# Optimization experiments

Hardware: AMD Instinct MI355X
Metric: run time of the kernel (lower is better)

The kernel has to match this reference:

```python
import jax, jax.numpy as jnp
import numpy as np

EPS = 1e-5

def mean_variance_norm(x):
    # x: [b, c, h, w]; per-(b,c) instance norm over spatial, unbiased var (torch default)
    b, c, h, w = x.shape
    xf = x.reshape(b, c, h * w)
    mean = xf.mean(axis=2)
    var = xf.var(axis=2, ddof=1) + EPS
    std = jnp.sqrt(var)
    return (x - mean[:, :, None, None]) / std[:, :, None, None]

def conv1x1(x, w, b):
    # w: [out_c, in_c], b: [out_c]
    return jnp.einsum('oc,bchw->bohw', w, x) + b[None, :, None, None]

def setup_inputs() -> dict:
    key = jax.random.key(0)
    ks = jax.random.split(key, 10)
    b, C, H, W = 4, 512, 64, 64
    content = jax.random.normal(ks[0], (b, C, H, W), dtype=jnp.float32)
    style = jax.random.normal(ks[1], (b, C, H, W), dtype=jnp.float32)
    def w_(k, o, i):
        return jax.random.normal(k, (o, i), dtype=jnp.float32) * 0.02
    def b_(k, o):
        return jax.random.normal(k, (o,), dtype=jnp.float32) * 0.02
    return {
        'content': content, 'style': style,
        'f_w': w_(ks[2], C, C), 'f_b': b_(ks[3], C),
        'g_w': w_(ks[4], C, C), 'g_b': b_(ks[5], C),
        'h_w': w_(ks[6], C, C), 'h_b': b_(ks[7], C),
        'out_w': w_(ks[8], C, C), 'out_b': b_(ks[9], C),
    }

def reference(content, style, f_w, f_b, g_w, g_b, h_w, h_b, out_w, out_b):
    b, C, h, w = content.shape
    F = conv1x1(mean_variance_norm(content), f_w, f_b)   # [b,C,h,w]
    G = conv1x1(mean_variance_norm(style), g_w, g_b)     # [b,C,hg,wg]
    H = conv1x1(style, h_w, h_b)                          # [b,C,hg,wg]
    # spatial <= max_sample, so no subsampling branch
    Gf = G.reshape(b, C, -1)                              # [b,C,M]
    Hf = H.reshape(b, C, -1)                              # [b,C,M]
    Ff = F.reshape(b, C, -1)                              # [b,C,N]
    S = jnp.einsum('bcn,bcm->bnm', Ff, Gf)                # [b,N,M]
    S = jax.nn.softmax(S, axis=-1)
    styled = jnp.einsum('bcm,bnm->bcn', Hf, S)            # [b,C,N]
    styled = styled.reshape(b, C, h, w)
    return conv1x1(styled, out_w, out_b)
```

## Files before the change

kernel.cpp:

```cpp
#include <hip/hip_runtime.h>
#include <hip/hip_bf16.h>

typedef _Float16 f16;
typedef __attribute__((ext_vector_type(8))) _Float16 half8;
typedef __attribute__((ext_vector_type(4))) _Float16 half4;
typedef __attribute__((ext_vector_type(4))) float f32x4;

#define AS1 __attribute__((address_space(1)))
#define AS3 __attribute__((address_space(3)))

constexpr int CH  = 512;
constexpr int NSP = 4096;
constexpr int NB  = 4;

#define VM8  asm volatile("s_waitcnt vmcnt(8)"  ::: "memory")
#define VM6  asm volatile("s_waitcnt vmcnt(6)"  ::: "memory")
#define VM4  asm volatile("s_waitcnt vmcnt(4)"  ::: "memory")
#define VM2  asm volatile("s_waitcnt vmcnt(2)"  ::: "memory")
#define VM0  asm volatile("s_waitcnt vmcnt(0)"  ::: "memory")
#define BARS do { __builtin_amdgcn_s_barrier(); asm volatile("" ::: "memory"); } while (0)
#define SP1  __builtin_amdgcn_s_setprio(1)
#define SP0  __builtin_amdgcn_s_setprio(0)

__device__ __forceinline__ void gload_lds16(const void* g, void* l) {
    __builtin_amdgcn_global_load_lds((const AS1 void*)g, (AS3 void*)l, 16, 0, 0);
}

__global__ void transpose_f16_kernel(const float* __restrict__ content, const float* __restrict__ style,
                                     f16* __restrict__ content_t, f16* __restrict__ style_t,
                                     float* __restrict__ raw)
{
    int b = blockIdx.z & 3, is_style = blockIdx.z >> 2;
    const float* src = (is_style ? style : content) + (size_t)b * CH * NSP;
    f16* dst = (is_style ? style_t : content_t) + (size_t)b * NSP * CH;
    int c0 = blockIdx.y * 64, n0 = blockIdx.x * 64;
    __shared__ f16 tile[64][72];
    int t = threadIdx.x;
    #pragma unroll
    for (int i = 0; i < 4; i++) {
        int idx = t + i*256;
        int cr = idx >> 4, n4 = (idx & 15) * 4;
        float4 v = *(const float4*)(src + (size_t)(c0+cr)*NSP + n0 + n4);
        tile[cr][n4+0] = (f16)v.x; tile[cr][n4+1] = (f16)v.y;
        tile[cr][n4+2] = (f16)v.z; tile[cr][n4+3] = (f16)v.w;
    }
    __syncthreads();
    {
        int row = t >> 2, seg = (t & 3) * 16;
        float s1 = 0.f, s2 = 0.f;
        #pragma unroll
        for (int j = 0; j < 16; j++) {
            float x = (float)tile[row][seg + j];
            s1 += x; s2 += x * x;
        }
        s1 += __shfl_down(s1, 2, 4); s1 += __shfl_down(s1, 1, 4);
        s2 += __shfl_down(s2, 2, 4); s2 += __shfl_down(s2, 1, 4);
        if ((t & 3) == 0) {
            int si = is_style * 2 * NB * CH + b * CH + c0 + row;
            atomicAdd(&raw[si], s1);
            atomicAdd(&raw[si + NB * CH], s2);
        }
    }
    int nr = t >> 2, seg = (t & 3) * 16;
    __align__(16) f16 out_v[16];
    #pragma unroll
    for (int j = 0; j < 16; j++) out_v[j] = tile[seg + j][nr];
    f16* dp = dst + (size_t)(n0+nr)*CH + c0 + seg;
    *(int4*)dp = ((int4*)out_v)[0];
    *(int4*)(dp + 8) = ((int4*)out_v)[1];
}

__global__ void effw_kernel(const float* __restrict__ fw, const float* __restrict__ fb,
                            const float* __restrict__ gw, const float* __restrict__ gb,
                            const float* __restrict__ hw, const float* __restrict__ ow,
                            const float* __restrict__ raw,
                            f16* __restrict__ fw_e, float* __restrict__ fb_e,
                            f16* __restrict__ gw_e, float* __restrict__ gb_e,
                            f16* __restrict__ hw_h, f16* __restrict__ ow_h)
{
    int o = blockIdx.x, b = blockIdx.y, mode = blockIdx.z, t = threadIdx.x;
    if (mode >= 2) {
        if (b != 0) return;
        const float* srcw = (mode == 2) ? hw : ow;
        f16* dstw = (mode == 2) ? hw_h : ow_h;
        for (int c = t; c < CH; c += 128) dstw[o*CH + c] = (f16)srcw[o*CH + c];
        return;
    }
    const float* w  = mode ? gw : fw;
    const float* rw = raw + (mode ? 2*NB*CH : 0);
    f16* we = mode ? gw_e : fw_e;
    float part = 0.f;
    for (int c = t; c < CH; c += 128) {
        float s1 = rw[b*CH + c], s2 = rw[NB*CH + b*CH + c];
        float mn = s1 * (1.f/NSP);
        float var = (s2 - (float)NSP*mn*mn) * (1.f/(NSP-1));
        float is = rsqrtf(var + 1e-5f);
        float wv = w[o*CH + c];
        we[((size_t)b*CH + o)*CH + c] = (f16)(wv * is);
        part += wv * mn * is;
    }
    #pragma unroll
    for (int off = 32; off; off >>= 1) part += __shfl_down(part, off);
    __shared__ float rr[2];
    if ((t & 63) == 0) rr[t >> 6] = part;
    __syncthreads();
    if (t == 0) (mode ? gb_e : fb_e)[b*CH + o] = (mode ? gb : fb)[o] - (rr[0] + rr[1]);
}

__global__ __launch_bounds__(256)
void conv3_kernel(const f16* __restrict__ fw_e, const float* __restrict__ fb_e,
                  const f16* __restrict__ gw_e, const float* __restrict__ gb_e,
                  const f16* __restrict__ hw_h, const float* __restrict__ h_b,
                  const f16* __restrict__ content_t, const f16* __restrict__ style_t,
                  f16* __restrict__ F_t, f16* __restrict__ G_t, f16* __restrict__ H_)
{
    const int T = gridDim.x;
    const int bid = blockIdx.x;
    const int tile = (bid & 7) * (T >> 3) + (bid >> 3);
    const int zz = tile >> 7, rem = tile & 127;
    const int mt = rem >> 5, nt = rem & 31;
    const int kind = zz >> 2, b = zz & 3;

    const f16* W; const float* bias; const f16* Xt; f16* Y;
    if (kind == 0)      { W = fw_e + (size_t)b*CH*CH; bias = fb_e + b*CH; Xt = content_t + (size_t)b*NSP*CH; Y = F_t + (size_t)b*NSP*CH; }
    else if (kind == 1) { W = gw_e + (size_t)b*CH*CH; bias = gb_e + b*CH; Xt = style_t + (size_t)b*NSP*CH; Y = G_t + (size_t)b*NSP*CH; }
    else                { W = hw_h;                    bias = h_b;         Xt = style_t + (size_t)b*NSP*CH; Y = H_ + (size_t)b*CH*NSP; }

    const int m0 = mt * 128, n0 = nt * 128;
    const int t = threadIdx.x, wave = t >> 6, lane = t & 63;
    const int l15 = lane & 15, l4 = lane >> 4;
    const int wm = (wave >> 1) * 64, wn = (wave & 1) * 64;

    __shared__ __align__(16) f16 Al[8192];
    __shared__ __align__(16) f16 Bl[8192];

    f32x4 acc[4][4] = {};

    for (int ks = 0; ks < CH/64; ks++) {
        const int kk = ks * 64;
        #pragma unroll
        for (int j = 0; j < 4; j++) {
            int L  = ((wave*4 + j)*64 + lane) * 16;
            int SL = L ^ (((L >> 7) & 7) << 4);
            int row = SL >> 7, seg = (SL & 127) >> 1;
            gload_lds16(W  + (size_t)(m0 + row)*CH + kk + seg, &Al[L >> 1]);
            gload_lds16(Xt + (size_t)(n0 + row)*CH + kk + seg, &Bl[L >> 1]);
        }
        VM0; BARS;
        #pragma unroll
        for (int kb = 0; kb < 2; kb++) {
            half8 a[4], bb[4];
            #pragma unroll
            for (int i = 0; i < 4; i++) {
                int ab = (wm + i*16 + l15)*128 + kb*64 + l4*16;
                ab ^= ((ab >> 7) & 7) << 4;
                a[i] = *(const half8*)&Al[ab >> 1];
                int bby = (wn + i*16 + l15)*128 + kb*64 + l4*16;
                bby ^= ((bby >> 7) & 7) << 4;
                bb[i] = *(const half8*)&Bl[bby >> 1];
            }
            #pragma unroll
            for (int i = 0; i < 4; i++)
                #pragma unroll
                for (int jj = 0; jj < 4; jj++)
                    acc[i][jj] = __builtin_amdgcn_mfma_f32_16x16x32_f16(a[i], bb[jj], acc[i][jj], 0, 0, 0);
        }
        BARS;
    }

    #pragma unroll
    for (int i = 0; i < 4; i++) {
        const int ob = m0 + wm + i*16 + l4*4;
        f32x4 bv = *(const f32x4*)(bias + ob);
        #pragma unroll
        for (int jj = 0; jj < 4; jj++) {
            const int n = n0 + wn + jj*16 + l15;
            f32x4 v = acc[i][jj];
            v[0] += bv[0]; v[1] += bv[1]; v[2] += bv[2]; v[3] += bv[3];
            if (kind < 2) {
                half4 pk; pk[0]=(f16)v[0]; pk[1]=(f16)v[1]; pk[2]=(f16)v[2]; pk[3]=(f16)v[3];
                *(half4*)(Y + (size_t)n * CH + ob) = pk;
            } else {
                #pragma unroll
                for (int r = 0; r < 4; r++) Y[(size_t)(ob + r) * NSP + n] = (f16)v[r];
            }
        }
    }
}

template<int MODE>
__global__ __launch_bounds__(256)
void gemm_kernel(const f16* __restrict__ W, long wstrideb,
                 const f16* __restrict__ Xt, long xstrideb,
                 const float* __restrict__ bias, long bstrideb,
                 void* __restrict__ Y, long ystrideb,
                 int K, long ostride)
{
    const int z = blockIdx.z;
    W    += (size_t)z * wstrideb;
    Xt   += (size_t)z * xstrideb;
    bias += (size_t)z * bstrideb;
    const int m0 = blockIdx.y * 128, n0 = blockIdx.x * 128;
    const int t = threadIdx.x, wave = t >> 6, lane = t & 63;
    const int l15 = lane & 15, l4 = lane >> 4;
    const int wm = (wave >> 1) * 64, wn = (wave & 1) * 64;

    __shared__ __align__(16) f16 Al[2][8192];
    __shared__ __align__(16) f16 Bl[2][8192];

    f32x4 acc[4][4] = {};

    auto stage = [&](int bufi, int kk) {
        #pragma unroll
        for (int j = 0; j < 4; j++) {
            int L  = ((wave*4 + j)*64 + lane) * 16;
            int SL = L ^ (((L >> 7) & 7) << 4);
            int row = SL >> 7, seg = (SL & 127) >> 1;
            gload_lds16(W  + (size_t)(m0 + row)*K + kk + seg, &Al[bufi][L >> 1]);
            gload_lds16(Xt + (size_t)(n0 + row)*K + kk + seg, &Bl[bufi][L >> 1]);
        }
    };

    const int nks = K >> 6;
    stage(0, 0);
    for (int ks = 0; ks < nks; ks++) {
        int bufi = ks & 1;
        if (ks < nks-1) { stage(bufi ^ 1, (ks + 1) * 64); VM8; }
        else            { VM0; }
        BARS;
        #pragma unroll
        for (int kb = 0; kb < 2; kb++) {
            half8 a[4], bb[4];
            #pragma unroll
            for (int i = 0; i < 4; i++) {
                int ab = (wm + i*16 + l15)*128 + kb*64 + l4*16;
                ab ^= ((ab >> 7) & 7) << 4;
                a[i] = *(const half8*)&Al[bufi][ab >> 1];
                int bby = (wn + i*16 + l15)*128 + kb*64 + l4*16;
                bby ^= ((bby >> 7) & 7) << 4;
                bb[i] = *(const half8*)&Bl[bufi][bby >> 1];
            }
            #pragma unroll
            for (int i = 0; i < 4; i++)
                #pragma unroll
                for (int jj = 0; jj < 4; jj++)
                    acc[i][jj] = __builtin_amdgcn_mfma_f32_16x16x32_f16(a[i], bb[jj], acc[i][jj], 0, 0, 0);
        }
        BARS;
    }

    #pragma unroll
    for (int i = 0; i < 4; i++) {
        const int ob = m0 + wm + i*16 + l4*4;
        f32x4 bv = *(const f32x4*)(bias + ob);
        #pragma unroll
        for (int jj = 0; jj < 4; jj++) {
            const int n = n0 + wn + jj*16 + l15;
            f32x4 v = acc[i][jj];
            v[0] += bv[0]; v[1] += bv[1]; v[2] += bv[2]; v[3] += bv[3];
            float* Yf = (float*)Y + (size_t)z * ystrideb;
            #pragma unroll
            for (int r = 0; r < 4; r++) Yf[(size_t)(ob + r) * ostride + n] = v[r];
        }
    }
}

template<int TPB, int NCT>
__global__ __launch_bounds__(256)
void gemm_att_kernel(const f16* __restrict__ W, long wstrideb,
                     const f16* __restrict__ Xt, long xstrideb,
                     f16* __restrict__ Y, long ystrideb,
                     int K, long ostride)
{
    const int T = gridDim.x;
    const int bid = blockIdx.x;
    const int tile = (bid & 7) * (T >> 3) + (bid >> 3);
    const int z = tile / TPB, rem = tile - z * TPB;
    const int mt = rem / NCT, nt = rem - mt * NCT;
    W  += (size_t)z * wstrideb;
    Xt += (size_t)z * xstrideb;
    f16* Yb = Y + (size_t)z * ystrideb;
    const int m0 = mt * 128, n0 = nt * 128;

    const int t = threadIdx.x, wave = t >> 6, lane = t & 63;
    const int l15 = lane & 15, l4 = lane >> 4;
    const int wm = (wave >> 1) * 64, wn = (wave & 1) * 64;

    __shared__ __align__(16) f16 Al[8192];
    __shared__ __align__(16) f16 Bl[8192];

    f32x4 acc[4][4] = {};

    const int nks = K >> 6;
    for (int ks = 0; ks < nks; ks++) {
        const int kk = ks * 64;
        #pragma unroll
        for (int j = 0; j < 4; j++) {
            int L  = ((wave*4 + j)*64 + lane) * 16;
            int SL = L ^ (((L >> 7) & 7) << 4);
            int row = SL >> 7, seg = (SL & 127) >> 1;
            gload_lds16(W  + (size_t)(m0 + row)*K + kk + seg, &Al[L >> 1]);
            gload_lds16(Xt + (size_t)(n0 + row)*K + kk + seg, &Bl[L >> 1]);
        }
        VM0; BARS;
        #pragma unroll
        for (int kb = 0; kb < 2; kb++) {
            half8 a[4], bb[4];
            #pragma unroll
            for (int i = 0; i < 4; i++) {
                int ab = (wm + i*16 + l15)*128 + kb*64 + l4*16;
                ab ^= ((ab >> 7) & 7) << 4;
                a[i] = *(const half8*)&Al[ab >> 1];
                int bby = (wn + i*16 + l15)*128 + kb*64 + l4*16;
                bby ^= ((bby >> 7) & 7) << 4;
                bb[i] = *(const half8*)&Bl[bby >> 1];
            }
            #pragma unroll
            for (int i = 0; i < 4; i++)
                #pragma unroll
                for (int jj = 0; jj < 4; jj++)
                    acc[i][jj] = __builtin_amdgcn_mfma_f32_16x16x32_f16(a[i], bb[jj], acc[i][jj], 0, 0, 0);
        }
        BARS;
    }

    #pragma unroll
    for (int i = 0; i < 4; i++) {
        const int ob = m0 + wm + i*16 + l4*4;
        #pragma unroll
        for (int jj = 0; jj < 4; jj++) {
            const int ncol = n0 + wn + jj*16 + l15;
            #pragma unroll
            for (int r = 0; r < 4; r++)
                Yb[(size_t)(ob + r) * ostride + ncol] = (f16)acc[i][jj][r];
        }
    }
}

template<int TPB, int NCT, int SPLITK>
__global__ __launch_bounds__(512)
void gemm256_kernel(const f16* __restrict__ W, long wstrideb,
                    const f16* __restrict__ Xt, long xstrideb,
                    f16* __restrict__ Y0, f16* __restrict__ Y1, long ystrideb,
                    int K, int kstride, long ostride)
{
    const int T = gridDim.x;
    const int bid = blockIdx.x;
    const int tile = (bid & 7) * (T >> 3) + (bid >> 3);
    int rem = tile, sp = 0;
    if constexpr (SPLITK == 2) { sp = tile / (NB * TPB); rem = tile - sp * NB * TPB; }
    const int z = rem / TPB; rem -= z * TPB;
    const int mt = rem / NCT, nt = rem - mt * NCT;
    const f16* Wb = W  + (size_t)z * wstrideb + (size_t)sp * K;
    const f16* Xb = Xt + (size_t)z * xstrideb + (size_t)sp * K;
    f16* Yb = ((SPLITK == 2 && sp) ? Y1 : Y0) + (size_t)z * ystrideb;
    const int m0 = mt * 256, n0 = nt * 256;

    const int t = threadIdx.x, lane = t & 63, wave = t >> 6;
    const int l15 = lane & 15, l4 = lane >> 4;
    const int wr = wave >> 2, wc = wave & 3;

    __shared__ __align__(16) f16 As[2][16384];
    __shared__ __align__(16) f16 Bs[2][16384];

    f32x4 acc[8][4] = {};

    auto stA = [&](int nbuf, int kk, int half, int q) {
        int L  = half*16384 + q*8192 + t*16;
        int SL = L ^ (((L >> 7) & 7) << 4);
        gload_lds16(Wb + (size_t)(m0 + (SL >> 7)) * kstride + kk + ((SL & 127) >> 1), &As[nbuf][L >> 1]);
    };
    auto stB = [&](int nbuf, int kk, int half, int q) {
        int L  = half*16384 + q*8192 + t*16;
        int SL = L ^ (((L >> 7) & 7) << 4);
        gload_lds16(Xb + (size_t)(n0 + (SL >> 7)) * kstride + kk + ((SL & 127) >> 1), &Bs[nbuf][L >> 1]);
    };
    auto ldA = [&](int buf, int i, int kb) {
        int L = (((i&3)*16) + wr*64 + ((i>>2)*128) + l15)*128 + kb*64 + l4*16;
        L ^= ((L >> 7) & 7) << 4;
        return *(const half8*)&As[buf][L >> 1];
    };
    auto ldB = [&](int buf, int j, int kb) {
        int L = (((j&1)*16) + wc*32 + ((j>>1)*128) + l15)*128 + kb*64 + l4*16;
        L ^= ((L >> 7) & 7) << 4;
        return *(const half8*)&Bs[buf][L >> 1];
    };

    const int nks = K >> 6;
    stA(0,0,0,0); stA(0,0,0,1);
    stB(0,0,0,0); stB(0,0,0,1);
    stB(0,0,1,0); stB(0,0,1,1);
    stA(0,0,1,0); stA(0,0,1,1);
    VM4;
    if (nks > 1) {
        stA(1,64,0,0); stA(1,64,0,1);
        stB(1,64,0,0); stB(1,64,0,1);
        stB(1,64,1,0); stB(1,64,1,1);
        VM6;
    } else { VM0; }
    BARS;

    half8 a[4][2], b01[2][2], b23[2][2];

    for (int kt = 0; kt < nks; kt++) {
        const int buf = kt & 1;
        const int kk1 = (kt+1) << 6, kk2 = (kt+2) << 6;
        const bool s1 = (kt+1 < nks), s2 = (kt+2 < nks);

        #pragma unroll
        for (int i = 0; i < 4; i++) { a[i][0] = ldA(buf, i, 0); a[i][1] = ldA(buf, i, 1); }
        #pragma unroll
        for (int j = 0; j < 2; j++) { b01[j][0] = ldB(buf, j, 0); b01[j][1] = ldB(buf, j, 1); }
        if (s1) { stA(buf^1, kk1, 1, 0); stA(buf^1, kk1, 1, 1); }
        else    { VM2; }
        BARS; SP1;
        #pragma unroll
        for (int i = 0; i < 4; i++)
            #pragma unroll
            for (int j = 0; j < 2; j++)
                #pragma unroll
                for (int kb = 0; kb < 2; kb++)
                    acc[i][j] = __builtin_amdgcn_mfma_f32_16x16x32_f16(a[i][kb], b01[j][kb], acc[i][j], 0, 0, 0);
        SP0; BARS;

        #pragma unroll
        for (int j = 0; j < 2; j++) { b23[j][0] = ldB(buf, 2+j, 0); b23[j][1] = ldB(buf, 2+j, 1); }
        if (s2)       { stA(buf, kk2, 0, 0); stA(buf, kk2, 0, 1); }
        else if (!s1) { VM0; }
        BARS; SP1;
        #pragma unroll
        for (int i = 0; i < 4; i++)
            #pragma unroll
            for (int j = 0; j < 2; j++)
                #pragma unroll
                for (int kb = 0; kb < 2; kb++)
                    acc[i][2+j] = __builtin_amdgcn_mfma_f32_16x16x32_f16(a[i][kb], b23[j][kb], acc[i][2+j], 0, 0, 0);
        SP0; BARS;

        #pragma unroll
        for (int i = 0; i < 4; i++) { a[i][0] = ldA(buf, 4+i, 0); a[i][1] = ldA(buf, 4+i, 1); }
        if (s2) { stB(buf, kk2, 0, 0); stB(buf, kk2, 0, 1); }
        BARS; SP1;
        #pragma unroll
        for (int i = 0; i < 4; i++)
            #pragma unroll
            for (int j = 0; j < 2; j++)
                #pragma unroll
                for (int kb = 0; kb < 2; kb++)
                    acc[4+i][2+j] = __builtin_amdgcn_mfma_f32_16x16x32_f16(a[i][kb], b23[j][kb], acc[4+i][2+j], 0, 0, 0);
        SP0; BARS;

        if (s2)      { stB(buf, kk2, 1, 0); stB(buf, kk2, 1, 1); VM6; }
        else if (s1) { VM4; }
        BARS; SP1;
        #pragma unroll
        for (int i = 0; i < 4; i++)
            #pragma unroll
            for (int j = 0; j < 2; j++)
                #pragma unroll
                for (int kb = 0; kb < 2; kb++)
                    acc[4+i][j] = __builtin_amdgcn_mfma_f32_16x16x32_f16(a[i][kb], b01[j][kb], acc[4+i][j], 0, 0, 0);
        SP0; BARS;
    }

    #pragma unroll
    for (int i = 0; i < 8; i++) {
        const int ob = m0 + ((i&3)*16) + wr*64 + ((i>>2)*128) + l4*4;
        #pragma unroll
        for (int j = 0; j < 4; j++) {
            const int ncol = n0 + ((j&1)*16) + wc*32 + ((j>>1)*128) + l15;
            f32x4 v = acc[i][j];
            #pragma unroll
            for (int r = 0; r < 4; r++)
                Yb[(size_t)(ob + r) * ostride + ncol] = (f16)v[r];
        }
    }
}

__global__ __launch_bounds__(256)
void reduce_pv_kernel(const f16* __restrict__ p0, const f16* __restrict__ p1, f16* __restrict__ out)
{
    size_t i = ((size_t)blockIdx.x * 256 + threadIdx.x) * 8;
    half8 a = *(const half8*)(p0 + i);
    half8 b = *(const half8*)(p1 + i);
    half8 o;
    #pragma unroll
    for (int e = 0; e < 8; e++) o[e] = (f16)((float)a[e] + (float)b[e]);
    *(half8*)(out + i) = o;
}

__global__ __launch_bounds__(256)
void softmax_kernel(f16* __restrict__ S, int nrows)
{
    int row = blockIdx.x * 4 + (threadIdx.x >> 6);
    if (row >= nrows) return;
    int lane = threadIdx.x & 63;
    f16* p = S + (size_t)row * NSP + lane * 8;

    half8 v[8];
    #pragma unroll
    for (int j = 0; j < 8; j++) v[j] = *(const half8*)(p + j * 512);

    float mx = -1e30f;
    #pragma unroll
    for (int j = 0; j < 8; j++)
        #pragma unroll
        for (int e = 0; e < 8; e++) mx = fmaxf(mx, (float)v[j][e]);
    #pragma unroll
    for (int off = 32; off; off >>= 1) mx = fmaxf(mx, __shfl_xor(mx, off));

    float ex[64];
    float s = 0.f;
    #pragma unroll
    for (int j = 0; j < 8; j++)
        #pragma unroll
        for (int e = 0; e < 8; e++) {
            float x = __expf((float)v[j][e] - mx);
            ex[j*8 + e] = x; s += x;
        }
    #pragma unroll
    for (int off = 32; off; off >>= 1) s += __shfl_xor(s, off);
    float inv = 1.0f / s;

    #pragma unroll
    for (int j = 0; j < 8; j++) {
        half8 o;
        #pragma unroll
        for (int e = 0; e < 8; e++) o[e] = (f16)(ex[j*8 + e] * inv);
        *(half8*)(p + j * 512) = o;
    }
}

extern "C" void kernel_launch(void* const* d_in, const int* in_sizes, int n_in,
                              void* d_out, int out_size, void* d_ws, size_t ws_size,
                              hipStream_t stream)
{
    const float* content = (const float*)d_in[0];
    const float* style   = (const float*)d_in[1];
    const float* f_w = (const float*)d_in[2];
    const float* f_b = (const float*)d_in[3];
    const float* g_w = (const float*)d_in[4];
    const float* g_b = (const float*)d_in[5];
    const float* h_w = (const float*)d_in[6];
    const float* h_b = (const float*)d_in[7];
    const float* o_w = (const float*)d_in[8];
    const float* o_b = (const float*)d_in[9];

    char* ws = (char*)d_ws;
    size_t off = 0;
    auto alloc = [&](size_t bytes) -> void* {
        void* p = ws + off;
        off += (bytes + 255) & ~(size_t)255;
        return p;
    };
    float* raw = (float*)alloc(4 * NB*CH * 4);
    f16* fw_e = (f16*)alloc((size_t)NB*CH*CH*2);
    f16* gw_e = (f16*)alloc((size_t)NB*CH*CH*2);
    f16* hw_h = (f16*)alloc((size_t)CH*CH*2);
    f16* ow_h = (f16*)alloc((size_t)CH*CH*2);
    float* fb_e = (float*)alloc((size_t)NB*CH*4);
    float* gb_e = (float*)alloc((size_t)NB*CH*4);
    f16* content_t = (f16*)alloc((size_t)NB*NSP*CH*2);
    f16* style_t   = (f16*)alloc((size_t)NB*NSP*CH*2);
    f16* F_t = (f16*)alloc((size_t)NB*NSP*CH*2);
    f16* G_t = (f16*)alloc((size_t)NB*NSP*CH*2);
    f16* H_  = (f16*)alloc((size_t)NB*CH*NSP*2);
    f16* styled_t = content_t;

    size_t s_plane = (size_t)NSP * NSP;
    bool all4 = (off + 4 * s_plane * 2 <= ws_size);
    f16* S16 = (f16*)alloc((all4 ? 4 : 1) * s_plane * 2);
    if (off > ws_size) return;

    hipMemsetAsync(raw, 0, 4 * NB*CH * 4, stream);
    transpose_f16_kernel<<<dim3(NSP/64, CH/64, NB*2), dim3(256), 0, stream>>>(
        content, style, content_t, style_t, raw);
    effw_kernel<<<dim3(CH, NB, 4), dim3(128), 0, stream>>>(f_w, f_b, g_w, g_b, h_w, o_w, raw,
                                                           fw_e, fb_e, gw_e, gb_e, hw_h, ow_h);
    conv3_kernel<<<dim3(12*128), dim3(256), 0, stream>>>(
        fw_e, fb_e, gw_e, gb_e, hw_h, h_b, content_t, style_t, F_t, G_t, H_);

    if (all4) {
        gemm256_kernel<256,16,1><<<dim3(1024), dim3(512), 0, stream>>>(
            F_t, (long)NSP*CH, G_t, (long)NSP*CH, S16, nullptr, (long)s_plane, CH, CH, (long)NSP);
        softmax_kernel<<<dim3(NB*NSP/4), dim3(256), 0, stream>>>(S16, NB*NSP);
        gemm256_kernel<32,2,2><<<dim3(256), dim3(512), 0, stream>>>(
            S16, (long)s_plane, H_, (long)CH*NSP, F_t, G_t, (long)NSP*CH, NSP/2, NSP, (long)CH);
        reduce_pv_kernel<<<dim3((int)((size_t)NB*NSP*CH/2048)), dim3(256), 0, stream>>>(F_t, G_t, styled_t);
    } else {
        for (int b = 0; b < NB; b++) {
            gemm_att_kernel<1024,32><<<dim3(1024), dim3(256), 0, stream>>>(
                F_t + (size_t)b*NSP*CH, 0L, G_t + (size_t)b*NSP*CH, 0L,
                S16, 0L, CH, (long)NSP);
            softmax_kernel<<<dim3(NSP/4), dim3(256), 0, stream>>>(S16, NSP);
            gemm_att_kernel<128,4><<<dim3(128), dim3(256), 0, stream>>>(
                S16, 0L, H_ + (size_t)b*CH*NSP, 0L,
                styled_t + (size_t)b*NSP*CH, 0L, NSP, (long)CH);
        }
    }

    gemm_kernel<2><<<dim3(NSP/128, CH/128, NB), dim3(256), 0, stream>>>(
        ow_h, 0L, styled_t, (long)NSP*CH, o_b, 0L, d_out, (long)CH*NSP, CH, (long)NSP);
}
```

Measured before the change: 291.6 us.

## Replace QK^T GEMM with 128x256 four-wave kernel writing transposed vectorized output

Adds a new attention-score GEMM kernel with 256-thread blocks and 128x256 tiles. It swaps the operand roles so G is the M side and F the N side, then writes S transposed with packed half4 stores instead of scalar stores. The goal is better store coalescing and a different occupancy and tiling balance for the S = F^T G product. The new kernel is single-buffered and waits on vmcnt(0) each k-step, so it gives up the load/compute overlap the previous kernel may have had.

```diff
diff --git a/kernel.cpp b/kernel.cpp
--- a/kernel.cpp
+++ b/kernel.cpp
@@ -333,6 +333,102 @@
             #pragma unroll
             for (int r = 0; r < 4; r++)
                 Yb[(size_t)(ob + r) * ostride + ncol] = (f16)acc[i][jj][r];
+        }
+    }
+}
+
+template<int TPB, int NCT, int SPLITK>
+__global__ __launch_bounds__(256)
+void gemm_att2_kernel(const f16* __restrict__ W, long wstrideb,
+                      const f16* __restrict__ Xt, long xstrideb,
+                      f16* __restrict__ Y0, f16* __restrict__ Y1, long ystrideb,
+                      int K, int kstride, long ostride)
+{
+    const int T = gridDim.x;
+    const int bid = blockIdx.x;
+    const int tile = (bid & 7) * (T >> 3) + (bid >> 3);
+    int rem = tile, sp = 0;
+    if constexpr (SPLITK == 2) { sp = tile / (NB * TPB); rem = tile - sp * NB * TPB; }
+    const int z = rem / TPB; rem -= z * TPB;
+    const int mt = rem / NCT, nt = rem - mt * NCT;
+    const f16* Wb = W  + (size_t)z * wstrideb + (size_t)sp * K;
+    const f16* Xb = Xt + (size_t)z * xstrideb + (size_t)sp * K;
+    f16* Yb = ((SPLITK == 2 && sp) ? Y1 : Y0) + (size_t)z * ystrideb;
+    const int m0 = mt * 128, n0 = nt * 256;
+
+    const int t = threadIdx.x, wave = t >> 6, lane = t & 63;
+    const int l15 = lane & 15, l4 = lane >> 4;
+    const int wn = wave * 64;
+
+    __shared__ __align__(16) f16 As[8192];
+    __shared__ __align__(16) f16 Bs[16384];
+
+    f32x4 acc[8][4] = {};
+
+    auto ldA = [&](int i, int kb) {
+        int L = (i*16 + l15)*128 + kb*64 + l4*16;
+        L ^= ((L >> 7) & 7) << 4;
+        return *(const half8*)&As[L >> 1];
+    };
+    auto ldB = [&](int j, int kb) {
+        int L = (wn + j*16 + l15)*128 + kb*64 + l4*16;
+        L ^= ((L >> 7) & 7) << 4;
+        return *(const half8*)&Bs[L >> 1];
+    };
+
+    const int nks = K >> 6;
+    for (int ks = 0; ks < nks; ks++) {
+        const int kk = ks * 64;
+        #pragma unroll
+        for (int q = 0; q < 4; q++) {
+            int L  = (q*256 + t) * 16;
+            int SL = L ^ (((L >> 7) & 7) << 4);
+            gload_lds16(Wb + (size_t)(m0 + (SL >> 7)) * kstride + kk + ((SL & 127) >> 1), &As[L >> 1]);
+        }
+        #pragma unroll
+        for (int q = 0; q < 8; q++) {
+            int L  = (q*256 + t) * 16;
+            int SL = L ^ (((L >> 7) & 7) << 4);
+            gload_lds16(Xb + (size_t)(n0 + (SL >> 7)) * kstride + kk + ((SL & 127) >> 1), &Bs[L >> 1]);
+        }
+        VM0; BARS;
+
+        half8 a[4][2], b[4][2];
+        #pragma unroll
+        for (int i = 0; i < 4; i++) { a[i][0] = ldA(i, 0); a[i][1] = ldA(i, 1); }
+        #pragma unroll
+        for (int j = 0; j < 4; j++) { b[j][0] = ldB(j, 0); b[j][1] = ldB(j, 1); }
+        SP1;
+        #pragma unroll
+        for (int i = 0; i < 4; i++)
+            #pragma unroll
+            for (int j = 0; j < 4; j++)
+                #pragma unroll
+                for (int kb = 0; kb < 2; kb++)
+                    acc[i][j] = __builtin_amdgcn_mfma_f32_16x16x32_f16(a[i][kb], b[j][kb], acc[i][j], 0, 0, 0);
+        SP0;
+        #pragma unroll
+        for (int i = 0; i < 4; i++) { a[i][0] = ldA(4+i, 0); a[i][1] = ldA(4+i, 1); }
+        SP1;
+        #pragma unroll
+        for (int i = 0; i < 4; i++)
+            #pragma unroll
+            for (int j = 0; j < 4; j++)
+                #pragma unroll
+                for (int kb = 0; kb < 2; kb++)
+                    acc[4+i][j] = __builtin_amdgcn_mfma_f32_16x16x32_f16(a[i][kb], b[j][kb], acc[4+i][j], 0, 0, 0);
+        SP0; BARS;
+    }
+
+    #pragma unroll
+    for (int i = 0; i < 8; i++) {
+        const int ob = m0 + i*16 + l4*4;
+        #pragma unroll
+        for (int j = 0; j < 4; j++) {
+            const int ncol = n0 + wn + j*16 + l15;
+            f32x4 v = acc[i][j];
+            half4 pk; pk[0]=(f16)v[0]; pk[1]=(f16)v[1]; pk[2]=(f16)v[2]; pk[3]=(f16)v[3];
+            *(half4*)(Yb + (size_t)ncol * ostride + ob) = pk;
         }
     }
 }
@@ -581,8 +677,8 @@
         fw_e, fb_e, gw_e, gb_e, hw_h, h_b, content_t, style_t, F_t, G_t, H_);
 
     if (all4) {
-        gemm256_kernel<256,16,1><<<dim3(1024), dim3(512), 0, stream>>>(
-            F_t, (long)NSP*CH, G_t, (long)NSP*CH, S16, nullptr, (long)s_plane, CH, CH, (long)NSP);
+        gemm_att2_kernel<512,16,1><<<dim3(2048), dim3(256), 0, stream>>>(
+            G_t, (long)NSP*CH, F_t, (long)NSP*CH, S16, nullptr, (long)s_plane, CH, CH, (long)NSP);
         softmax_kernel<<<dim3(NB*NSP/4), dim3(256), 0, stream>>>(S16, NB*NSP);
         gemm256_kernel<32,2,2><<<dim3(256), dim3(512), 0, stream>>>(
             S16, (long)s_plane, H_, (long)CH*NSP, F_t, G_t, (long)NSP*CH, NSP/2, NSP, (long)CH);
```

Measured after the change: 366.9 us. 1.26x slower.

## Fuse split-K partial sum into output conv GEMM and transpose QK^T store

Applied to the files above, without the earlier changes.

Removes the separate reduce kernel that summed the two split-K partials of the PV GEMM; the output 1x1 conv GEMM now loads both partials, adds them in registers and stages the sum into LDS. The QK^T GEMM swaps its operands and, in a new mode, stores half4 vectors along the contiguous dimension, so the S layout is unchanged but stores are wider. This saves one kernel launch and one full round trip of the styled tensor through memory. The fused kernel loads its B operand through registers instead of direct-to-LDS loads and has no software pipelining, which may slow the output GEMM.

```diff
diff --git a/kernel.cpp b/kernel.cpp
--- a/kernel.cpp
+++ b/kernel.cpp
@@ -265,6 +265,81 @@
     }
 }
 
+__global__ __launch_bounds__(256)
+void out_fused_kernel(const f16* __restrict__ W, const f16* __restrict__ P0, const f16* __restrict__ P1,
+                      const float* __restrict__ bias, float* __restrict__ Y)
+{
+    const int z = blockIdx.z;
+    const f16* p0 = P0 + (size_t)z * NSP * CH;
+    const f16* p1 = P1 + (size_t)z * NSP * CH;
+    float* Yf = Y + (size_t)z * CH * NSP;
+    const int m0 = blockIdx.y * 128, n0 = blockIdx.x * 128;
+    const int t = threadIdx.x, wave = t >> 6, lane = t & 63;
+    const int l15 = lane & 15, l4 = lane >> 4;
+    const int wm = (wave >> 1) * 64, wn = (wave & 1) * 64;
+
+    __shared__ __align__(16) f16 Al[8192];
+    __shared__ __align__(16) f16 Bl[8192];
+
+    f32x4 acc[4][4] = {};
+
+    for (int ks = 0; ks < CH/64; ks++) {
+        const int kk = ks * 64;
+        int Ls[4];
+        half8 b0[4], b1[4];
+        #pragma unroll
+        for (int j = 0; j < 4; j++) {
+            int L  = ((wave*4 + j)*64 + lane) * 16;
+            int SL = L ^ (((L >> 7) & 7) << 4);
+            int row = SL >> 7, seg = (SL & 127) >> 1;
+            gload_lds16(W + (size_t)(m0 + row)*CH + kk + seg, &Al[L >> 1]);
+            b0[j] = *(const half8*)(p0 + (size_t)(n0 + row)*CH + kk + seg);
+            b1[j] = *(const half8*)(p1 + (size_t)(n0 + row)*CH + kk + seg);
+            Ls[j] = L;
+        }
+        #pragma unroll
+        for (int j = 0; j < 4; j++) {
+            half8 s;
+            #pragma unroll
+            for (int e = 0; e < 8; e++) s[e] = (f16)((float)b0[j][e] + (float)b1[j][e]);
+            *(half8*)&Bl[Ls[j] >> 1] = s;
+        }
+        __syncthreads();
+        #pragma unroll
+        for (int kb = 0; kb < 2; kb++) {
+            half8 a[4], bb[4];
+            #pragma unroll
+            for (int i = 0; i < 4; i++) {
+                int ab = (wm + i*16 + l15)*128 + kb*64 + l4*16;
+                ab ^= ((ab >> 7) & 7) << 4;
+                a[i] = *(const half8*)&Al[ab >> 1];
+                int bby = (wn + i*16 + l15)*128 + kb*64 + l4*16;
+                bby ^= ((bby >> 7) & 7) << 4;
+                bb[i] = *(const half8*)&Bl[bby >> 1];
+            }
+            #pragma unroll
+            for (int i = 0; i < 4; i++)
+                #pragma unroll
+                for (int jj = 0; jj < 4; jj++)
+                    acc[i][jj] = __builtin_amdgcn_mfma_f32_16x16x32_f16(a[i], bb[jj], acc[i][jj], 0, 0, 0);
+        }
+        __syncthreads();
+    }
+
+    #pragma unroll
+    for (int i = 0; i < 4; i++) {
+        const int ob = m0 + wm + i*16 + l4*4;
+        f32x4 bv = *(const f32x4*)(bias + ob);
+        #pragma unroll
+        for (int jj = 0; jj < 4; jj++) {
+            const int n = n0 + wn + jj*16 + l15;
+            f32x4 v = acc[i][jj];
+            #pragma unroll
+            for (int r = 0; r < 4; r++) Yf[(size_t)(ob + r) * NSP + n] = v[r] + bv[r];
+        }
+    }
+}
+
 template<int TPB, int NCT>
 __global__ __launch_bounds__(256)
 void gemm_att_kernel(const f16* __restrict__ W, long wstrideb,
@@ -337,7 +412,7 @@
     }
 }
 
-template<int TPB, int NCT, int SPLITK>
+template<int TPB, int NCT, int SPLITK, int MODET = 0>
 __global__ __launch_bounds__(512)
 void gemm256_kernel(const f16* __restrict__ W, long wstrideb,
                     const f16* __restrict__ Xt, long xstrideb,
@@ -470,23 +545,16 @@
         for (int j = 0; j < 4; j++) {
             const int ncol = n0 + ((j&1)*16) + wc*32 + ((j>>1)*128) + l15;
             f32x4 v = acc[i][j];
-            #pragma unroll
-            for (int r = 0; r < 4; r++)
-                Yb[(size_t)(ob + r) * ostride + ncol] = (f16)v[r];
-        }
-    }
-}
-
-__global__ __launch_bounds__(256)
-void reduce_pv_kernel(const f16* __restrict__ p0, const f16* __restrict__ p1, f16* __restrict__ out)
-{
-    size_t i = ((size_t)blockIdx.x * 256 + threadIdx.x) * 8;
-    half8 a = *(const half8*)(p0 + i);
-    half8 b = *(const half8*)(p1 + i);
-    half8 o;
-    #pragma unroll
-    for (int e = 0; e < 8; e++) o[e] = (f16)((float)a[e] + (float)b[e]);
-    *(half8*)(out + i) = o;
+            if constexpr (MODET) {
+                half4 pk; pk[0]=(f16)v[0]; pk[1]=(f16)v[1]; pk[2]=(f16)v[2]; pk[3]=(f16)v[3];
+                *(half4*)(Yb + (size_t)ncol * ostride + ob) = pk;
+            } else {
+                #pragma unroll
+                for (int r = 0; r < 4; r++)
+                    Yb[(size_t)(ob + r) * ostride + ncol] = (f16)v[r];
+            }
+        }
+    }
 }
 
 __global__ __launch_bounds__(256)
@@ -581,12 +649,13 @@
         fw_e, fb_e, gw_e, gb_e, hw_h, h_b, content_t, style_t, F_t, G_t, H_);
 
     if (all4) {
-        gemm256_kernel<256,16,1><<<dim3(1024), dim3(512), 0, stream>>>(
-            F_t, (long)NSP*CH, G_t, (long)NSP*CH, S16, nullptr, (long)s_plane, CH, CH, (long)NSP);
+        gemm256_kernel<256,16,1,1><<<dim3(1024), dim3(512), 0, stream>>>(
+            G_t, (long)NSP*CH, F_t, (long)NSP*CH, S16, nullptr, (long)s_plane, CH, CH, (long)NSP);
         softmax_kernel<<<dim3(NB*NSP/4), dim3(256), 0, stream>>>(S16, NB*NSP);
         gemm256_kernel<32,2,2><<<dim3(256), dim3(512), 0, stream>>>(
             S16, (long)s_plane, H_, (long)CH*NSP, F_t, G_t, (long)NSP*CH, NSP/2, NSP, (long)CH);
-        reduce_pv_kernel<<<dim3((int)((size_t)NB*NSP*CH/2048)), dim3(256), 0, stream>>>(F_t, G_t, styled_t);
+        out_fused_kernel<<<dim3(NSP/128, CH/128, NB), dim3(256), 0, stream>>>(
+            ow_h, F_t, G_t, o_b, (float*)d_out);
     } else {
         for (int b = 0; b < NB; b++) {
             gemm_att_kernel<1024,32><<<dim3(1024), dim3(256), 0, stream>>>(
@@ -597,8 +666,7 @@
                 S16, 0L, H_ + (size_t)b*CH*NSP, 0L,
                 styled_t + (size_t)b*NSP*CH, 0L, NSP, (long)CH);
         }
-    }
-
-    gemm_kernel<2><<<dim3(NSP/128, CH/128, NB), dim3(256), 0, stream>>>(
-        ow_h, 0L, styled_t, (long)NSP*CH, o_b, 0L, d_out, (long)CH*NSP, CH, (long)NSP);
-}
+        gemm_kernel<2><<<dim3(NSP/128, CH/128, NB), dim3(256), 0, stream>>>(
+            ow_h, 0L, styled_t, (long)NSP*CH, o_b, 0L, d_out, (long)CH*NSP, CH, (long)NSP);
+    }
+}
```

Result: slower. 297.9 us (+2.2%).
